# Kernel optimization log

Hardware: AMD Instinct MI355X
Metric: run time of the kernel (lower is better)

## Reference

```python
import jax, jax.numpy as jnp
import numpy as np

N, R, M, E, NE, B = 50000, 500, 120000, 960000, 800000, 8192
D, H1, HID, OC = 200, 256, 512, 50


def setup_inputs() -> dict:
    key = jax.random.key(0)
    ks = jax.random.split(key, 26)
    s = 0.05
    rn = lambda k, shp: jax.random.normal(k, shp, jnp.float32) * s
    return {
        "entity_emb": jax.random.normal(ks[0], (N, D), jnp.float32),
        "rel_emb": jax.random.normal(ks[1], (R, D), jnp.float32),
        "b_x": jax.random.randint(ks[2], (M,), 0, N),
        "b_node_graph_index": jax.random.randint(ks[3], (M,), 0, R),
        "edge_src": jax.random.randint(ks[4], (E,), 0, M),
        "edge_dst": jax.random.randint(ks[5], (E,), 0, M),
        "edge_w": jax.random.uniform(ks[6], (E,), jnp.float32),
        "big_src": jax.random.randint(ks[7], (NE,), 0, N),
        "big_dst": jax.random.randint(ks[8], (NE,), 0, N),
        "big_w": jax.random.uniform(ks[9], (NE,), jnp.float32),
        "perm": jax.random.permutation(ks[10], N),
        "batch_inputs": jnp.stack([
            jax.random.randint(ks[11], (B,), 0, N),
            jax.random.randint(ks[12], (B,), 0, R),
            jax.random.randint(ks[13], (B,), 0, N)], axis=1),
        "W1a": rn(ks[14], (2 * D, H1)), "W1b": rn(ks[15], (H1, D)),
        "W2a": rn(ks[16], (D, H1)), "W2b": rn(ks[17], (H1, D)),
        "Wle": rn(ks[18], (2 * D, 1)), "ble": jnp.zeros((1,), jnp.float32),
        "Wlo": rn(ks[19], (2 * D, D)), "blo": jnp.zeros((D,), jnp.float32),
        "Wg": rn(ks[20], (D, HID)), "Wd": rn(ks[21], (HID, HID)),
        "conv_w": rn(ks[22], (OC, 3)), "conv_b": jnp.zeros((OC,), jnp.float32),
        "fc_w": rn(ks[23], (OC * D, 1)), "fc_b": jnp.zeros((1,), jnp.float32),
    }


def _l2norm(x):
    return x / jnp.maximum(jnp.linalg.norm(x, axis=-1, keepdims=True), 1e-12)


def _gcn(x, src, dst, w, n, Wa, Wb):
    # two-layer GCN over sparse edge list: out = A @ relu(A @ x @ Wa) @ Wb
    agg = lambda h: jax.ops.segment_sum(h[src] * w[:, None], dst, num_segments=n)
    h = jax.nn.relu(agg(x) @ Wa)
    return agg(h) @ Wb


def _seg_softmax(v, idx, n):
    m = jax.ops.segment_max(v, idx, num_segments=n)
    e = jnp.exp(v - m[idx])
    s = jax.ops.segment_sum(e, idx, num_segments=n)
    return e / (s[idx] + 1e-16)


def _mce(ent, rel, b_x, b_gi, src, dst, w, W1a, W1b, Wle, ble, Wlo, blo):
    x = jnp.concatenate([ent[b_x], rel[b_gi]], axis=-1)          # [M, 400]
    e = _gcn(x, src, dst, w, b_x.shape[0], W1a, W1b)             # [M, 200]
    cnt = jax.ops.segment_sum(jnp.ones((b_x.shape[0],), e.dtype), b_x, num_segments=N)
    mean = jax.ops.segment_sum(e, b_x, num_segments=N) / jnp.maximum(cnt, 1.0)[:, None]
    z = mean[b_x]                                                # scatter_mean then gather
    emb = jnp.concatenate([e[b_x], z], axis=-1)                  # [M, 400]
    score = emb @ Wle + ble                                      # [M, 1]
    zs = _seg_softmax(score, b_x, N)                             # segment softmax
    pooled = jax.ops.segment_sum(zs * emb, b_x, num_segments=N)  # [N, 400]
    return (pooled @ Wlo + blo) + ent


def _dgi(h1, h2, Wg, Wd):
    p1 = jax.nn.relu(h1 @ Wg)
    p2 = jax.nn.relu(h2 @ Wg)
    c = jax.nn.sigmoid(jnp.mean(p1, axis=0))                     # readout [HID]
    t = Wd @ c
    return jnp.concatenate([p1 @ t, p2 @ t])                     # [2N]


def _convkb(trip, conv_w, conv_b, fc_w, fc_b):
    # trip [B,3,D]; Conv2d(1, OC, (1,3)) over [B,1,D,3] -> [B,OC,D]
    h = jax.nn.relu(jnp.einsum('bsd,os->bod', trip, conv_w) + conv_b[None, :, None])
    return h.reshape(trip.shape[0], -1) @ fc_w + fc_b            # [B,1]


def reference(entity_emb, rel_emb, b_x, b_node_graph_index, edge_src, edge_dst,
              edge_w, big_src, big_dst, big_w, perm, batch_inputs,
              W1a, W1b, W2a, W2b, Wle, ble, Wlo, blo, Wg, Wd,
              conv_w, conv_b, fc_w, fc_b):
    ent = _l2norm(entity_emb)
    rel = _l2norm(rel_emb)
    ent_shuf = ent[perm]
    ec = _mce(ent, rel, b_x, b_node_graph_index, edge_src, edge_dst, edge_w,
              W1a, W1b, Wle, ble, Wlo, blo)
    ec_ = _mce(ent_shuf, rel, b_x, b_node_graph_index, edge_src, edge_dst, edge_w,
               W1a, W1b, Wle, ble, Wlo, blo)
    eg = _gcn(ec, big_src, big_dst, big_w, N, W2a, W2b)
    eg_ = _gcn(ec_, big_src, big_dst, big_w, N, W2a, W2b)
    local_logits = _dgi(ec, ec_, Wg, Wd)
    global_logits = _dgi(eg, eg_, Wg, Wd)
    trip = jnp.stack([ec[batch_inputs[:, 0]], rel[batch_inputs[:, 1]],
                      ec[batch_inputs[:, 2]]], axis=1)           # [B,3,D]
    out_conv = _convkb(trip, conv_w, conv_b, fc_w, fc_b)
    return out_conv, local_logits, global_logits
```

## Files before the change

### kernel.cpp

```cpp
#include <hip/hip_runtime.h>

#define NN   50000
#define RR   500
#define MM   120000
#define EE   960000
#define NEE  800000
#define BB   8192
#define DD   200
#define HH1  256
#define HIDD 512
#define OCC  50

typedef unsigned int  u32;
typedef unsigned short u16;
typedef __attribute__((ext_vector_type(8))) short bf16x8;
typedef __attribute__((ext_vector_type(4))) float f32x4;

static __device__ __forceinline__ float bf2f(u16 u) {
    u32 x = ((u32)u) << 16;
    return __uint_as_float(x);
}
static __device__ __forceinline__ u16 f2bf(float f) {
    u32 x = __float_as_uint(f);
    u32 r = (x + 0x7FFFu + ((x >> 16) & 1u)) >> 16;
    return (u16)r;
}
static __device__ __forceinline__ u32 pack2(float a, float b) {
    return (u32)f2bf(a) | ((u32)f2bf(b) << 16);
}
static __device__ __forceinline__ void unpack2(u32 v, float& a, float& b) {
    a = bf2f((u16)(v & 0xFFFFu));
    b = bf2f((u16)(v >> 16));
}

static __device__ __forceinline__ float wredsum(float v) {
#pragma unroll
    for (int off = 32; off > 0; off >>= 1) v += __shfl_xor(v, off);
    return v;
}

static __device__ __forceinline__ u32 relu2bf(u32 x) {
    if (x & 0x00008000u) x &= 0xFFFF0000u;
    if (x & 0x80000000u) x &= 0x0000FFFFu;
    return x;
}
static __device__ __forceinline__ bf16x8 zero8() {
    bf16x8 z;
#pragma unroll
    for (int i = 0; i < 8; ++i) z[i] = 0;
    return z;
}

__global__ void k_l2norm(const float* __restrict__ in, float* __restrict__ outf,
                         u16* __restrict__ outb, int rows) {
    int w = (blockIdx.x * blockDim.x + threadIdx.x) >> 6;
    int lane = threadIdx.x & 63;
    if (w >= rows) return;
    const float* r = in + (size_t)w * DD;
    float s = 0.f;
    for (int d = lane; d < DD; d += 64) { float v = r[d]; s += v * v; }
    s = wredsum(s);
    float inv = 1.0f / fmaxf(sqrtf(s), 1e-12f);
    for (int d = lane; d < DD; d += 64) {
        float v = r[d] * inv;
        if (outf) outf[(size_t)w * DD + d] = v;
        if (outb) outb[(size_t)w * DD + d] = f2bf(v);
    }
}

__global__ void k_gather_perm(const int* __restrict__ bx, const int* __restrict__ perm,
                              int* __restrict__ idx1, int M) {
    int m = blockIdx.x * blockDim.x + threadIdx.x;
    if (m < M) idx1[m] = perm[bx[m]];
}

__global__ void k_edge_idx(const int* __restrict__ srcE, const int* __restrict__ map,
                           int* __restrict__ outE, int n) {
    int e = blockIdx.x * blockDim.x + threadIdx.x;
    if (e < n) outE[e] = map[srcE[e]];
}

__global__ void k_prepw(const float* __restrict__ src, int Nc, int Kd,
                        u16* __restrict__ hi, u16* __restrict__ lo) {
    int i = blockIdx.x * blockDim.x + threadIdx.x;
    if (i >= Nc * Kd) return;
    int n = i / Kd, k = i - n * Kd;
    float b = src[(size_t)k * Nc + n];
    u16 hb_ = f2bf(b);
    hi[i] = hb_;
    lo[i] = f2bf(b - bf2f(hb_));
}

__global__ void k_fusew(const float* __restrict__ W2b, const float* __restrict__ Wg,
                        u16* __restrict__ hi, u16* __restrict__ lo) {
    int i = blockIdx.x * blockDim.x + threadIdx.x;
    if (i >= HIDD * HH1) return;
    int n = i >> 8, k = i & 255;
    float s = 0.f;
    for (int j = 0; j < DD; ++j) s += W2b[k * DD + j] * Wg[(size_t)j * HIDD + n];
    u16 h = f2bf(s);
    hi[i] = h;
    lo[i] = f2bf(s - bf2f(h));
}

__global__ void k_hist(const int* __restrict__ idx, int* __restrict__ cnt, int n) {
    int i = blockIdx.x * blockDim.x + threadIdx.x;
    if (i < n) atomicAdd(&cnt[idx[i]], 1);
}

__global__ __launch_bounds__(1024) void k_scan3(
    const int* __restrict__ in0, int* __restrict__ out0, int n0,
    const int* __restrict__ in1, int* __restrict__ out1, int n1,
    const int* __restrict__ in2, int* __restrict__ out2, int n2) {
    __shared__ int wtot[16];
    __shared__ int wexc[16];
    __shared__ int s_carry;
    const int* in = (blockIdx.x == 0) ? in0 : (blockIdx.x == 1) ? in1 : in2;
    int* out = (blockIdx.x == 0) ? out0 : (blockIdx.x == 1) ? out1 : out2;
    int n = (blockIdx.x == 0) ? n0 : (blockIdx.x == 1) ? n1 : n2;
    int tid = threadIdx.x, lane = tid & 63, wid = tid >> 6;
    if (tid == 0) s_carry = 0;
    __syncthreads();
    for (int base = 0; base < n; base += 1024) {
        int i = base + tid;
        int v = (i < n) ? in[i] : 0;
        int x = v;
#pragma unroll
        for (int off = 1; off < 64; off <<= 1) {
            int t = __shfl_up(x, off);
            if (lane >= off) x += t;
        }
        if (lane == 63) wtot[wid] = x;
        __syncthreads();
        if (wid == 0) {
            int wv2 = (lane < 16) ? wtot[lane] : 0;
            int y = wv2;
#pragma unroll
            for (int off = 1; off < 16; off <<= 1) {
                int t = __shfl_up(y, off);
                if (lane >= off) y += t;
            }
            if (lane < 16) wexc[lane] = y - wv2;
            if (lane == 15) wtot[15] = y;
        }
        __syncthreads();
        if (i < n) out[i] = s_carry + wexc[wid] + (x - v);
        int chunk_total = wtot[15];
        __syncthreads();
        if (tid == 0) s_carry += chunk_total;
        __syncthreads();
    }
    if (threadIdx.x == 0) out[n] = s_carry;
}

__global__ void k_fill2(const int* __restrict__ dst, const int* __restrict__ src,
                        const float* __restrict__ w, int* __restrict__ cursor,
                        int* __restrict__ srcs_out, float* __restrict__ ws_out, int n) {
    int e = blockIdx.x * blockDim.x + threadIdx.x;
    if (e >= n) return;
    int p = atomicAdd(&cursor[dst[e]], 1);
    srcs_out[p] = src[e];
    ws_out[p] = w[e];
}

__global__ void k_fill1(const int* __restrict__ idx, int* __restrict__ cursor,
                        int* __restrict__ outm, int n) {
    int m = blockIdx.x * blockDim.x + threadIdx.x;
    if (m >= n) return;
    int p = atomicAdd(&cursor[idx[m]], 1);
    outm[p] = m;
}

__global__ void k_pull_mce(const int* __restrict__ rp, const int* __restrict__ ivE,
                           const int* __restrict__ giE, const float* __restrict__ wE,
                           const u16* __restrict__ Pent, const u16* __restrict__ Prel,
                           u16* __restrict__ out, int ndst) {
    int wv = (blockIdx.x * blockDim.x + threadIdx.x) >> 6;
    if (wv >= ndst) return;
    int lane = threadIdx.x & 63;
    int beg = rp[wv], end = rp[wv + 1];
    float accA[2] = {0.f, 0.f}, accB[2] = {0.f, 0.f};
    int e = beg;
    for (; e + 4 <= end; e += 4) {
        int i0 = ivE[e], i1 = ivE[e + 1], i2 = ivE[e + 2], i3 = ivE[e + 3];
        int g0 = giE[e], g1 = giE[e + 1], g2 = giE[e + 2], g3 = giE[e + 3];
        float w0 = wE[e], w1 = wE[e + 1], w2 = wE[e + 2], w3 = wE[e + 3];
        const u32* pe0 = (const u32*)(Pent + (size_t)i0 * HH1);
        const u32* pe1 = (const u32*)(Pent + (size_t)i1 * HH1);
        const u32* pe2 = (const u32*)(Pent + (size_t)i2 * HH1);
        const u32* pe3 = (const u32*)(Pent + (size_t)i3 * HH1);
        const u32* pr0 = (const u32*)(Prel + (size_t)g0 * HH1);
        const u32* pr1 = (const u32*)(Prel + (size_t)g1 * HH1);
        const u32* pr2 = (const u32*)(Prel + (size_t)g2 * HH1);
        const u32* pr3 = (const u32*)(Prel + (size_t)g3 * HH1);
        u32 vp[4][2], vr[4][2];
#pragma unroll
        for (int t = 0; t < 2; ++t) {
            int p = lane + 64 * t;
            vp[0][t] = pe0[p]; vp[1][t] = pe1[p]; vp[2][t] = pe2[p]; vp[3][t] = pe3[p];
            vr[0][t] = pr0[p]; vr[1][t] = pr1[p]; vr[2][t] = pr2[p]; vr[3][t] = pr3[p];
        }
#pragma unroll
        for (int t = 0; t < 2; ++t) {
            float a, b, c, d;
            unpack2(vp[0][t], a, b); unpack2(vr[0][t], c, d);
            accA[t] += (a + c) * w0; accB[t] += (b + d) * w0;
            unpack2(vp[1][t], a, b); unpack2(vr[1][t], c, d);
            accA[t] += (a + c) * w1; accB[t] += (b + d) * w1;
            unpack2(vp[2][t], a, b); unpack2(vr[2][t], c, d);
            accA[t] += (a + c) * w2; accB[t] += (b + d) * w2;
            unpack2(vp[3][t], a, b); unpack2(vr[3][t], c, d);
            accA[t] += (a + c) * w3; accB[t] += (b + d) * w3;
        }
    }
    for (; e < end; ++e) {
        int iv = ivE[e], gi = giE[e];
        float w = wE[e];
        const u32* pe = (const u32*)(Pent + (size_t)iv * HH1);
        const u32* pr = (const u32*)(Prel + (size_t)gi * HH1);
#pragma unroll
        for (int t = 0; t < 2; ++t) {
            int p = lane + 64 * t;
            float a, b, c, d;
            unpack2(pe[p], a, b); unpack2(pr[p], c, d);
            accA[t] += (a + c) * w; accB[t] += (b + d) * w;
        }
    }
    u32* o = (u32*)(out + (size_t)wv * HH1);
#pragma unroll
    for (int t = 0; t < 2; ++t) o[lane + 64 * t] = pack2(accA[t], accB[t]);
}

template<int DIMS, int INS, int OUTS>
__global__ void k_pull(const int* __restrict__ rp, const int* __restrict__ srcs,
                       const float* __restrict__ wsrt,
                       const u16* __restrict__ inh, const u16* __restrict__ inl,
                       u16* __restrict__ outh, u16* __restrict__ outl, int ndst) {
    int wv = (blockIdx.x * blockDim.x + threadIdx.x) >> 6;
    if (wv >= ndst) return;
    int lane = threadIdx.x & 63;
    int beg = rp[wv], end = rp[wv + 1];
    constexpr int NP = DIMS / 2;
    constexpr int NT = (NP + 63) / 64;
    float accA[NT], accB[NT];
#pragma unroll
    for (int t = 0; t < NT; ++t) { accA[t] = 0.f; accB[t] = 0.f; }
    int e = beg;
    for (; e + 4 <= end; e += 4) {
        int s0 = srcs[e], s1 = srcs[e + 1], s2 = srcs[e + 2], s3 = srcs[e + 3];
        float w0 = wsrt[e], w1 = wsrt[e + 1], w2 = wsrt[e + 2], w3 = wsrt[e + 3];
        const u32* rh[4] = {
            (const u32*)(inh + (size_t)s0 * DIMS), (const u32*)(inh + (size_t)s1 * DIMS),
            (const u32*)(inh + (size_t)s2 * DIMS), (const u32*)(inh + (size_t)s3 * DIMS)};
        u32 vh[4][NT], vl[4][NT];
#pragma unroll
        for (int t = 0; t < NT; ++t) {
            int p = lane + 64 * t;
            if (p < NP) {
                vh[0][t] = rh[0][p]; vh[1][t] = rh[1][p];
                vh[2][t] = rh[2][p]; vh[3][t] = rh[3][p];
            }
        }
        if (INS) {
            const u32* rl[4] = {
                (const u32*)(inl + (size_t)s0 * DIMS), (const u32*)(inl + (size_t)s1 * DIMS),
                (const u32*)(inl + (size_t)s2 * DIMS), (const u32*)(inl + (size_t)s3 * DIMS)};
#pragma unroll
            for (int t = 0; t < NT; ++t) {
                int p = lane + 64 * t;
                if (p < NP) {
                    vl[0][t] = rl[0][p]; vl[1][t] = rl[1][p];
                    vl[2][t] = rl[2][p]; vl[3][t] = rl[3][p];
                }
            }
        }
        float ws[4] = {w0, w1, w2, w3};
#pragma unroll
        for (int q = 0; q < 4; ++q) {
#pragma unroll
            for (int t = 0; t < NT; ++t) {
                int p = lane + 64 * t;
                if (p < NP) {
                    float a, b;
                    unpack2(vh[q][t], a, b);
                    if (INS) { float a2, b2; unpack2(vl[q][t], a2, b2); a += a2; b += b2; }
                    accA[t] += a * ws[q]; accB[t] += b * ws[q];
                }
            }
        }
    }
    for (; e < end; ++e) {
        int s = srcs[e];
        float w = wsrt[e];
        const u32* rh = (const u32*)(inh + (size_t)s * DIMS);
        const u32* rl = INS ? (const u32*)(inl + (size_t)s * DIMS) : nullptr;
#pragma unroll
        for (int t = 0; t < NT; ++t) {
            int p = lane + 64 * t;
            if (p < NP) {
                float a, b;
                unpack2(rh[p], a, b);
                if (INS) { float a2, b2; unpack2(rl[p], a2, b2); a += a2; b += b2; }
                accA[t] += a * w; accB[t] += b * w;
            }
        }
    }
    u32* oh = (u32*)(outh + (size_t)wv * DIMS);
    u32* ol = OUTS ? (u32*)(outl + (size_t)wv * DIMS) : nullptr;
#pragma unroll
    for (int t = 0; t < NT; ++t) {
        int p = lane + 64 * t;
        if (p < NP) {
            if (OUTS == 0) {
                oh[p] = pack2(accA[t], accB[t]);
            } else {
                u16 ha = f2bf(accA[t]), hb_ = f2bf(accB[t]);
                u16 la = f2bf(accA[t] - bf2f(ha)), lb = f2bf(accB[t] - bf2f(hb_));
                oh[p] = (u32)ha | ((u32)hb_ << 16);
                ol[p] = (u32)la | ((u32)lb << 16);
            }
        }
    }
}

__global__ void k_segpool(const int* __restrict__ rpX, const int* __restrict__ mids,
                          const u16* __restrict__ e_buf, u16* __restrict__ pooled, int n) {
    int nv = (blockIdx.x * blockDim.x + threadIdx.x) >> 6;
    if (nv >= n) return;
    int lane = threadIdx.x & 63;
    int beg = rpX[nv], end = rpX[nv + 1];
    int cnt = end - beg;
    float accA[2] = {0.f, 0.f}, accB[2] = {0.f, 0.f};
    int e = beg;
    for (; e + 4 <= end; e += 4) {
        const u32* r0 = (const u32*)(e_buf + (size_t)mids[e] * DD);
        const u32* r1 = (const u32*)(e_buf + (size_t)mids[e + 1] * DD);
        const u32* r2 = (const u32*)(e_buf + (size_t)mids[e + 2] * DD);
        const u32* r3 = (const u32*)(e_buf + (size_t)mids[e + 3] * DD);
        u32 v[4][2];
#pragma unroll
        for (int t = 0; t < 2; ++t) {
            int p = lane + 64 * t;
            if (p < DD / 2) { v[0][t] = r0[p]; v[1][t] = r1[p]; v[2][t] = r2[p]; v[3][t] = r3[p]; }
        }
#pragma unroll
        for (int t = 0; t < 2; ++t) {
            int p = lane + 64 * t;
            if (p < DD / 2) {
                float a, b;
                unpack2(v[0][t], a, b); accA[t] += a; accB[t] += b;
                unpack2(v[1][t], a, b); accA[t] += a; accB[t] += b;
                unpack2(v[2][t], a, b); accA[t] += a; accB[t] += b;
                unpack2(v[3][t], a, b); accA[t] += a; accB[t] += b;
            }
        }
    }
    for (; e < end; ++e) {
        const u32* r = (const u32*)(e_buf + (size_t)mids[e] * DD);
#pragma unroll
        for (int t = 0; t < 2; ++t) {
            int p = lane + 64 * t;
            if (p < DD / 2) { float a, b; unpack2(r[p], a, b); accA[t] += a; accB[t] += b; }
        }
    }
    float inv = 1.0f / fmaxf((float)cnt, 1.0f);
    bool occ = cnt > 0;
    const u32* er = (const u32*)(e_buf + (size_t)nv * DD);
    u32* p0 = (u32*)(pooled + (size_t)nv * (2 * DD));
#pragma unroll
    for (int t = 0; t < 2; ++t) {
        int p = lane + 64 * t;
        if (p < DD / 2) {
            p0[p] = occ ? er[p] : 0u;
            p0[DD / 2 + p] = occ ? pack2(accA[t] * inv, accB[t] * inv) : 0u;
        }
    }
}

template<int AMODE, int BLO, int RELU_IN, int RELU_OUT, int HAS_BIAS, int HAS_ADD, int FUSE, int CMODE>
__global__ __launch_bounds__(256) void k_mfmamm(
    const u16* __restrict__ Ah, const u16* __restrict__ Al,
    const u16* __restrict__ Bh, const u16* __restrict__ Bl,
    void* __restrict__ Cv, u16* __restrict__ Cl,
    int Mr, int Nc, int Kd, int redrows,
    const float* __restrict__ bias, const u16* __restrict__ addsrc,
    const int* __restrict__ addidx, const float* __restrict__ tvec,
    float* __restrict__ redout) {
    constexpr int BM = 128, BK = 32;
    constexpr int ASTR = 40;
    __shared__ u16 Ahs[2][BM * ASTR];
    __shared__ u16 Als[AMODE ? 2 : 1][AMODE ? (BM * ASTR) : 8];

    int tid = threadIdx.x;
    int wid = tid >> 6, lane = tid & 63;
    int wr = wid >> 1, wc = wid & 1;
    int r = lane & 15, h = lane >> 4;
    int bm0 = blockIdx.y * BM, bn0 = blockIdx.x * 128;
    int srow = (tid & 15) + 16 * (tid >> 6);
    int sg = (tid >> 4) & 3;
    int nk = (Kd + BK - 1) / BK;

    f32x4 acc[4][4];
#pragma unroll
    for (int i = 0; i < 4; ++i)
#pragma unroll
        for (int j = 0; j < 4; ++j) acc[i][j] = (f32x4){0.f, 0.f, 0.f, 0.f};

    uint4 pa[2], pl[2];
    {
        int kc = sg * 8;
        bool kok = (kc + 8 <= Kd);
#pragma unroll
        for (int it = 0; it < 2; ++it) {
            int row = srow + 64 * it;
            int gr = bm0 + row;
            uint4 v = make_uint4(0, 0, 0, 0), vl2 = make_uint4(0, 0, 0, 0);
            if (gr < Mr && kok) {
                v = *(const uint4*)(Ah + (size_t)gr * Kd + kc);
                if (AMODE) vl2 = *(const uint4*)(Al + (size_t)gr * Kd + kc);
            }
            if (RELU_IN) {
                v.x = relu2bf(v.x); v.y = relu2bf(v.y);
                v.z = relu2bf(v.z); v.w = relu2bf(v.w);
            }
            pa[it] = v;
            if (AMODE) pl[it] = vl2;
        }
#pragma unroll
        for (int it = 0; it < 2; ++it) {
            int row = srow + 64 * it;
            *(uint4*)(&Ahs[0][row * ASTR + sg * 8]) = pa[it];
            if (AMODE) *(uint4*)(&Als[0][row * ASTR + sg * 8]) = pl[it];
        }
    }
    __syncthreads();

    for (int k = 0; k < nk; ++k) {
        int cur = k & 1;
        uint4 na[2], nl[2];
        bool have_next = (k + 1 < nk);
        if (have_next) {
            int kc = (k + 1) * BK + sg * 8;
            bool kok = (kc + 8 <= Kd);
#pragma unroll
            for (int it = 0; it < 2; ++it) {
                int row = srow + 64 * it;
                int gr = bm0 + row;
                uint4 v = make_uint4(0, 0, 0, 0), vl2 = make_uint4(0, 0, 0, 0);
                if (gr < Mr && kok) {
                    v = *(const uint4*)(Ah + (size_t)gr * Kd + kc);
                    if (AMODE) vl2 = *(const uint4*)(Al + (size_t)gr * Kd + kc);
                }
                if (RELU_IN) {
                    v.x = relu2bf(v.x); v.y = relu2bf(v.y);
                    v.z = relu2bf(v.z); v.w = relu2bf(v.w);
                }
                na[it] = v;
                if (AMODE) nl[it] = vl2;
            }
        }
        bf16x8 bh4[4], bl4[4];
        {
            int kb = k * BK + h * 8;
            bool kbok = (kb + 8 <= Kd);
#pragma unroll
            for (int j = 0; j < 4; ++j) {
                int nrow = bn0 + wc * 64 + j * 16 + r;
                if (nrow < Nc && kbok) {
                    bh4[j] = *(const bf16x8*)(Bh + (size_t)nrow * Kd + kb);
                    if (BLO) bl4[j] = *(const bf16x8*)(Bl + (size_t)nrow * Kd + kb);
                } else { bh4[j] = zero8(); if (BLO) bl4[j] = zero8(); }
            }
        }
        bf16x8 af[4], alr[4];
#pragma unroll
        for (int i = 0; i < 4; ++i) {
            int mrow = wr * 64 + i * 16 + r;
            af[i] = *(const bf16x8*)(&Ahs[cur][mrow * ASTR + h * 8]);
            if (AMODE) alr[i] = *(const bf16x8*)(&Als[cur][mrow * ASTR + h * 8]);
        }
#pragma unroll
        for (int i = 0; i < 4; ++i)
#pragma unroll
            for (int j = 0; j < 4; ++j) {
                acc[i][j] = __builtin_amdgcn_mfma_f32_16x16x32_bf16(af[i], bh4[j], acc[i][j], 0, 0, 0);
                if (BLO)
                    acc[i][j] = __builtin_amdgcn_mfma_f32_16x16x32_bf16(af[i], bl4[j], acc[i][j], 0, 0, 0);
                if (AMODE)
                    acc[i][j] = __builtin_amdgcn_mfma_f32_16x16x32_bf16(alr[i], bh4[j], acc[i][j], 0, 0, 0);
            }
        if (have_next) {
#pragma unroll
            for (int it = 0; it < 2; ++it) {
                int row = srow + 64 * it;
                *(uint4*)(&Ahs[cur ^ 1][row * ASTR + sg * 8]) = na[it];
                if (AMODE) *(uint4*)(&Als[cur ^ 1][row * ASTR + sg * 8]) = nl[it];
            }
        }
        __syncthreads();
    }
    float colacc[4] = {0.f, 0.f, 0.f, 0.f};
#pragma unroll
    for (int i = 0; i < 4; ++i) {
        float rowacc[4] = {0.f, 0.f, 0.f, 0.f};
#pragma unroll
        for (int j = 0; j < 4; ++j) {
            int col = bn0 + wc * 64 + j * 16 + r;
            bool colok = col < Nc;
            float tv = (FUSE == 2 && colok) ? tvec[col] : 0.f;
#pragma unroll
            for (int rg = 0; rg < 4; ++rg) {
                int row = bm0 + wr * 64 + i * 16 + h * 4 + rg;
                float v = acc[i][j][rg];
                if (HAS_BIAS && colok) v += bias[col];
                if (RELU_OUT) v = fmaxf(v, 0.f);
                bool ok = colok && row < Mr;
                if (HAS_ADD && ok) {
                    int r2 = addidx ? addidx[row] : row;
                    v += bf2f(addsrc[(size_t)r2 * Nc + col]);
                }
                if (FUSE != 2 && ok) {
                    size_t cidx = (size_t)row * Nc + col;
                    if (CMODE == 0) ((u16*)Cv)[cidx] = f2bf(v);
                    else if (CMODE == 1) ((float*)Cv)[cidx] = v;
                    else {
                        u16 hi_ = f2bf(v);
                        ((u16*)Cv)[cidx] = hi_;
                        Cl[cidx] = f2bf(v - bf2f(hi_));
                    }
                }
                if (FUSE == 1 && ok && row < redrows) colacc[j] += v;
                if (FUSE == 2) rowacc[rg] += v * tv;
            }
        }
        if (FUSE == 2) {
#pragma unroll
            for (int rg = 0; rg < 4; ++rg) {
                float val = rowacc[rg];
                val += __shfl_xor(val, 1); val += __shfl_xor(val, 2);
                val += __shfl_xor(val, 4); val += __shfl_xor(val, 8);
                int row = bm0 + wr * 64 + i * 16 + h * 4 + rg;
                if (r == 0 && row < Mr) atomicAdd(&redout[row], val);
            }
        }
    }
    if (FUSE == 1) {
#pragma unroll
        for (int j = 0; j < 4; ++j) {
            float val = colacc[j];
            val += __shfl_xor(val, 16); val += __shfl_xor(val, 32);
            int col = bn0 + wc * 64 + j * 16 + r;
            if (h == 0 && col < Nc) atomicAdd(&redout[col], val);
        }
    }
}

__global__ void k_tmv(const float* __restrict__ Wd, const float* __restrict__ csum,
                      float* __restrict__ tvec) {
    __shared__ float c[HIDD];
    int lane = threadIdx.x;
    for (int j = lane; j < HIDD; j += 64)
        c[j] = 1.0f / (1.0f + expf(-csum[j] * (1.0f / (float)NN)));
    __syncthreads();
    int r0 = blockIdx.x * 16;
    for (int i = r0; i < r0 + 16; ++i) {
        const float* wr = Wd + (size_t)i * HIDD;
        float s = 0.f;
        for (int j = lane; j < HIDD; j += 64) s += wr[j] * c[j];
        s = wredsum(s);
        if (lane == 0) tvec[i] = s;
    }
}

__global__ void k_rowdot512(const float* __restrict__ p, const float* __restrict__ t,
                            float* __restrict__ out, int rows) {
    int g = blockIdx.x * blockDim.x + threadIdx.x;
    int wv = g >> 6;
    if (wv >= rows) return;
    int lane = g & 63;
    const float* r = p + (size_t)wv * HIDD;
    float s = 0.f;
#pragma unroll
    for (int t4 = 0; t4 < 8; ++t4) {
        int d = lane + t4 * 64;
        s += r[d] * t[d];
    }
    s = wredsum(s);
    if (lane == 0) out[wv] = s;
}

__global__ void k_rowdot512b(const u16* __restrict__ p, const float* __restrict__ t,
                             float* __restrict__ out, int rows) {
    int g = blockIdx.x * blockDim.x + threadIdx.x;
    int wv = g >> 6;
    if (wv >= rows) return;
    int lane = g & 63;
    const u32* r = (const u32*)(p + (size_t)wv * HIDD);
    float s = 0.f;
#pragma unroll
    for (int t4 = 0; t4 < 4; ++t4) {
        int pp = lane + t4 * 64;
        float a, b;
        unpack2(r[pp], a, b);
        s += a * t[2 * pp] + b * t[2 * pp + 1];
    }
    s = wredsum(s);
    if (lane == 0) out[wv] = s;
}

__global__ void k_convkb(const u16* __restrict__ ec, const float* __restrict__ rel,
                         const int* __restrict__ bi, const float* __restrict__ cw,
                         const float* __restrict__ cb, const float* __restrict__ fcw,
                         const float* __restrict__ fcb, float* __restrict__ out) {
    __shared__ float t0[DD], t1[DD], t2[DD];
    __shared__ float red[4];
    int b = blockIdx.x, tid = threadIdx.x;
    int i0 = bi[b * 3 + 0], i1 = bi[b * 3 + 1], i2 = bi[b * 3 + 2];
    if (tid < DD) {
        t0[tid] = bf2f(ec[(size_t)i0 * DD + tid]);
        t1[tid] = rel[(size_t)i1 * DD + tid];
        t2[tid] = bf2f(ec[(size_t)i2 * DD + tid]);
    }
    __syncthreads();
    float partial = 0.f;
    if (tid < DD) {
        float a = t0[tid], bb = t1[tid], c = t2[tid];
        for (int o = 0; o < OCC; ++o) {
            float h = fmaxf(cw[o * 3 + 0] * a + cw[o * 3 + 1] * bb + cw[o * 3 + 2] * c + cb[o], 0.f);
            partial += h * fcw[o * DD + tid];
        }
    }
    partial = wredsum(partial);
    if ((tid & 63) == 0) red[tid >> 6] = partial;
    __syncthreads();
    if (tid == 0) out[b] = red[0] + red[1] + red[2] + red[3] + fcb[0];
}

__global__ void k_sentinel(float* out, float val) { out[threadIdx.x] = val; }

extern "C" void kernel_launch(void* const* d_in, const int* in_sizes, int n_in,
                              void* d_out, int out_size, void* d_ws, size_t ws_size,
                              hipStream_t stream) {
    const float* entity_emb = (const float*)d_in[0];
    const float* rel_emb    = (const float*)d_in[1];
    const int*   b_x        = (const int*)d_in[2];
    const int*   b_gi       = (const int*)d_in[3];
    const int*   e_src      = (const int*)d_in[4];
    const int*   e_dst      = (const int*)d_in[5];
    const float* e_w        = (const float*)d_in[6];
    const int*   big_src    = (const int*)d_in[7];
    const int*   big_dst    = (const int*)d_in[8];
    const float* big_w      = (const float*)d_in[9];
    const int*   perm       = (const int*)d_in[10];
    const int*   batch_in   = (const int*)d_in[11];
    const float* W1a        = (const float*)d_in[12];
    const float* W1b        = (const float*)d_in[13];
    const float* W2a        = (const float*)d_in[14];
    const float* W2b        = (const float*)d_in[15];
    const float* Wlo        = (const float*)d_in[18];
    const float* blo        = (const float*)d_in[19];
    const float* Wg         = (const float*)d_in[20];
    const float* Wd         = (const float*)d_in[21];
    const float* conv_w     = (const float*)d_in[22];
    const float* conv_b     = (const float*)d_in[23];
    const float* fc_w       = (const float*)d_in[24];
    const float* fc_b       = (const float*)d_in[25];
    float* out = (float*)d_out;

    size_t off = 0;
    auto balloc = [&](size_t nbytes) {
        size_t p = off;
        off += (nbytes + 511) & ~(size_t)511;
        return p;
    };
    char* base = (char*)d_ws;
    u16*   entb = (u16*)(base + balloc((size_t)NN * DD * 2));
    float* relf = (float*)(base + balloc((size_t)RR * DD * 4));
    u16*   relb = (u16*)(base + balloc((size_t)RR * DD * 2));
    u16*   Pent = (u16*)(base + balloc((size_t)NN * HH1 * 2));
    u16*   Prel = (u16*)(base + balloc((size_t)RR * HH1 * 2));
    int*   idx1 = (int*)(base + balloc((size_t)MM * 4));
    int*   rpB  = (int*)(base + balloc((size_t)(NN + 1) * 4));
    int*   srcB = (int*)(base + balloc((size_t)NEE * 4));
    float* wB   = (float*)(base + balloc((size_t)NEE * 4));
    int*   rpE  = (int*)(base + balloc((size_t)(MM + 1) * 4));
    int*   srcE = (int*)(base + balloc((size_t)EE * 4));
    float* wE   = (float*)(base + balloc((size_t)EE * 4));
    int*   ivE  = (int*)(base + balloc((size_t)EE * 4));
    int*   giE  = (int*)(base + balloc((size_t)EE * 4));
    int*   rpX  = (int*)(base + balloc((size_t)(NN + 1) * 4));
    int*   mids = (int*)(base + balloc((size_t)MM * 4));
    int*   curB = (int*)(base + balloc((size_t)NN * 4));
    int*   curE = (int*)(base + balloc((size_t)MM * 4));
    int*   curX = (int*)(base + balloc((size_t)NN * 4));
    u16* w1aT_h  = (u16*)(base + balloc(200 * 256 * 2));
    u16* w1aT_l  = (u16*)(base + balloc(200 * 256 * 2));
    u16* w1abT_h = (u16*)(base + balloc(200 * 256 * 2));
    u16* w1abT_l = (u16*)(base + balloc(200 * 256 * 2));
    u16* w1bT_h  = (u16*)(base + balloc(256 * 200 * 2));
    u16* w1bT_l  = (u16*)(base + balloc(256 * 200 * 2));
    u16* wloT_h  = (u16*)(base + balloc(400 * 200 * 2));
    u16* wloT_l  = (u16*)(base + balloc(400 * 200 * 2));
    u16* wgT_h   = (u16*)(base + balloc(200 * 512 * 2));
    u16* wgT_l   = (u16*)(base + balloc(200 * 512 * 2));
    u16* w2aT_h  = (u16*)(base + balloc(200 * 256 * 2));
    u16* w2aT_l  = (u16*)(base + balloc(200 * 256 * 2));
    u16* w2bgT_h = (u16*)(base + balloc(512 * 256 * 2));
    u16* w2bgT_l = (u16*)(base + balloc(512 * 256 * 2));
    char*  Aarena = base + balloc((size_t)MM * HH1 * 2);
    char*  Barena = base + balloc((size_t)MM * DD * 2);
    char*  Carena = base + balloc((size_t)MM * DD * 2);
    float* csum = (float*)(base + balloc(4 * 2048));
    float* cvec = csum + 512;
    float* t_l  = csum + 1024;
    float* t_g  = csum + 1536;
    u16*   ecb  = (u16*)(base + balloc((size_t)NN * DD * 2));
    size_t off_small = off;
    u16*   ecb2 = ecb + (size_t)NN * DD;
    bool bigws = (off_small + (size_t)NN * DD * 2) <= ws_size;
    (void)cvec;

    if (ws_size < off_small) {
        k_sentinel<<<dim3(1), dim3(8), 0, stream>>>(out, (float)(ws_size >> 20));
        return;
    }

    const size_t PL = 20000000;
    const size_t PH = 25600000;
    u16*   aggx   = (u16*)Aarena;
    u16*   hb     = (u16*)Barena;
    u16*   e_buf  = (u16*)Carena;
    u16*   pooled = (u16*)Aarena;
    u16*   a1h    = (u16*)Aarena;
    u16*   a1l    = (u16*)(Aarena + PL);
    u16*   h2h    = (u16*)Barena;
    u16*   h2l    = (u16*)(Barena + PH);
    u16*   g2h    = (u16*)Aarena;
    u16*   g2l    = (u16*)(Aarena + PH);
    u16*   pb16   = (u16*)Barena;
    u16*   pb16L  = (u16*)Aarena;
    float* pbuf   = (float*)Aarena;

    dim3 blk(256);
    auto wgrid = [](int items) { return dim3((unsigned)((items + 3) / 4)); };
    auto tgrid = [](int items) { return dim3((unsigned)((items + 255) / 256)); };
    auto mmgrid = [](int Mr, int Nc) { return dim3((unsigned)((Nc + 127) / 128), (unsigned)((Mr + 127) / 128)); };

    k_l2norm<<<wgrid(NN), blk, 0, stream>>>(entity_emb, nullptr, entb, NN);
    k_l2norm<<<wgrid(RR), blk, 0, stream>>>(rel_emb, relf, relb, RR);
    k_gather_perm<<<tgrid(MM), blk, 0, stream>>>(b_x, perm, idx1, MM);
    k_prepw<<<tgrid(256 * 200), blk, 0, stream>>>(W1a, 256, 200, w1aT_h, w1aT_l);
    k_prepw<<<tgrid(256 * 200), blk, 0, stream>>>(W1a + 200 * 256, 256, 200, w1abT_h, w1abT_l);
    k_prepw<<<tgrid(200 * 256), blk, 0, stream>>>(W1b, 200, 256, w1bT_h, w1bT_l);
    k_prepw<<<tgrid(200 * 400), blk, 0, stream>>>(Wlo, 200, 400, wloT_h, wloT_l);
    k_prepw<<<tgrid(512 * 200), blk, 0, stream>>>(Wg, 512, 200, wgT_h, wgT_l);
    k_prepw<<<tgrid(256 * 200), blk, 0, stream>>>(W2a, 256, 200, w2aT_h, w2aT_l);
    k_fusew<<<tgrid(512 * 256), blk, 0, stream>>>(W2b, Wg, w2bgT_h, w2bgT_l);

    hipMemsetAsync(curB, 0, (size_t)NN * 4, stream);
    hipMemsetAsync(curE, 0, (size_t)MM * 4, stream);
    hipMemsetAsync(curX, 0, (size_t)NN * 4, stream);
    k_hist<<<tgrid(NEE), blk, 0, stream>>>(big_dst, curB, NEE);
    k_hist<<<tgrid(EE), blk, 0, stream>>>(e_dst, curE, EE);
    k_hist<<<tgrid(MM), blk, 0, stream>>>(b_x, curX, MM);
    k_scan3<<<dim3(3), dim3(1024), 0, stream>>>(curB, rpB, NN, curE, rpE, MM, curX, rpX, NN);
    hipMemcpyAsync(curB, rpB, (size_t)NN * 4, hipMemcpyDeviceToDevice, stream);
    hipMemcpyAsync(curE, rpE, (size_t)MM * 4, hipMemcpyDeviceToDevice, stream);
    hipMemcpyAsync(curX, rpX, (size_t)NN * 4, hipMemcpyDeviceToDevice, stream);
    k_fill2<<<tgrid(NEE), blk, 0, stream>>>(big_dst, big_src, big_w, curB, srcB, wB, NEE);
    k_fill2<<<tgrid(EE), blk, 0, stream>>>(e_dst, e_src, e_w, curE, srcE, wE, EE);
    k_fill1<<<tgrid(MM), blk, 0, stream>>>(b_x, curX, mids, MM);
    k_edge_idx<<<tgrid(EE), blk, 0, stream>>>(srcE, b_gi, giE, EE);

    k_mfmamm<0, 0, 0, 0, 0, 0, 0, 0><<<mmgrid(NN, HH1), blk, 0, stream>>>(
        entb, nullptr, w1aT_h, w1aT_l, Pent, nullptr, NN, HH1, DD, NN,
        nullptr, nullptr, nullptr, nullptr, nullptr);
    k_mfmamm<0, 0, 0, 0, 0, 0, 0, 0><<<mmgrid(RR, HH1), blk, 0, stream>>>(
        relb, nullptr, w1abT_h, w1abT_l, Prel, nullptr, RR, HH1, DD, RR,
        nullptr, nullptr, nullptr, nullptr, nullptr);

    auto mce_pass = [&](int v, u16* ecdst) {
        const int* ivmap  = v ? idx1 : b_x;
        const int* addidx = v ? perm : nullptr;
        k_edge_idx<<<tgrid(EE), blk, 0, stream>>>(srcE, ivmap, ivE, EE);
        k_pull_mce<<<wgrid(MM), blk, 0, stream>>>(rpE, ivE, giE, wE, Pent, Prel, aggx, MM);
        k_mfmamm<0, 0, 1, 0, 0, 0, 0, 0><<<mmgrid(MM, DD), blk, 0, stream>>>(
            aggx, nullptr, w1bT_h, w1bT_l, hb, nullptr, MM, DD, HH1, MM,
            nullptr, nullptr, nullptr, nullptr, nullptr);
        k_pull<DD, 0, 0><<<wgrid(MM), blk, 0, stream>>>(rpE, srcE, wE, hb, nullptr,
                                                        e_buf, nullptr, MM);
        k_segpool<<<wgrid(NN), blk, 0, stream>>>(rpX, mids, e_buf, pooled, NN);
        k_mfmamm<0, 0, 0, 0, 1, 1, 0, 0><<<mmgrid(NN, DD), blk, 0, stream>>>(
            pooled, nullptr, wloT_h, wloT_l, ecdst, nullptr, NN, DD, 2 * DD, NN,
            blo, entb, addidx, nullptr, nullptr);
    };

    auto gcn_pass = [&](int v, const u16* ecsrc) {
        k_pull<DD, 0, 1><<<wgrid(NN), blk, 0, stream>>>(rpB, srcB, wB, ecsrc, nullptr,
                                                        a1h, a1l, NN);
        k_mfmamm<1, 1, 0, 1, 0, 0, 0, 2><<<mmgrid(NN, HH1), blk, 0, stream>>>(
            a1h, a1l, w2aT_h, w2aT_l, h2h, h2l, NN, HH1, DD, NN,
            nullptr, nullptr, nullptr, nullptr, nullptr);
        k_pull<HH1, 1, 1><<<wgrid(NN), blk, 0, stream>>>(rpB, srcB, wB, h2h, h2l,
                                                         g2h, g2l, NN);
        if (v == 0) {
            hipMemsetAsync(csum, 0, 512 * sizeof(float), stream);
            k_mfmamm<1, 1, 0, 1, 0, 0, 1, 0><<<mmgrid(NN, HIDD), blk, 0, stream>>>(
                g2h, g2l, w2bgT_h, w2bgT_l, pb16, nullptr, NN, HIDD, HH1, NN,
                nullptr, nullptr, nullptr, nullptr, csum);
            k_tmv<<<dim3(32), dim3(64), 0, stream>>>(Wd, csum, t_g);
            k_rowdot512b<<<wgrid(NN), blk, 0, stream>>>(pb16, t_g, out + BB + 2 * (size_t)NN, NN);
        } else {
            hipMemsetAsync(out + BB + 3 * (size_t)NN, 0, (size_t)NN * 4, stream);
            k_mfmamm<1, 1, 0, 1, 0, 0, 2, 0><<<mmgrid(NN, HIDD), blk, 0, stream>>>(
                g2h, g2l, w2bgT_h, w2bgT_l, nullptr, nullptr, NN, HIDD, HH1, NN,
                nullptr, nullptr, nullptr, t_g, out + BB + 3 * (size_t)NN);
        }
    };

    if (bigws) {
        mce_pass(0, ecb);
        mce_pass(1, ecb2);
        hipMemsetAsync(csum, 0, 512 * sizeof(float), stream);
        k_mfmamm<0, 0, 0, 1, 0, 0, 1, 0><<<mmgrid(2 * NN, HIDD), blk, 0, stream>>>(
            ecb, nullptr, wgT_h, wgT_l, pb16L, nullptr, 2 * NN, HIDD, DD, NN,
            nullptr, nullptr, nullptr, nullptr, csum);
        k_tmv<<<dim3(32), dim3(64), 0, stream>>>(Wd, csum, t_l);
        k_rowdot512b<<<wgrid(2 * NN), blk, 0, stream>>>(pb16L, t_l, out + BB, 2 * NN);
        k_convkb<<<dim3(BB), blk, 0, stream>>>(ecb, relf, batch_in,
                                               conv_w, conv_b, fc_w, fc_b, out);
        gcn_pass(0, ecb);
        gcn_pass(1, ecb2);
    } else {
        for (int v = 0; v < 2; ++v) {
            mce_pass(v, ecb);
            if (v == 0) {
                hipMemsetAsync(csum, 0, 512 * sizeof(float), stream);
                k_mfmamm<0, 0, 0, 1, 0, 0, 1, 1><<<mmgrid(NN, HIDD), blk, 0, stream>>>(
                    ecb, nullptr, wgT_h, wgT_l, pbuf, nullptr, NN, HIDD, DD, NN,
                    nullptr, nullptr, nullptr, nullptr, csum);
                k_tmv<<<dim3(32), dim3(64), 0, stream>>>(Wd, csum, t_l);
                k_rowdot512<<<wgrid(NN), blk, 0, stream>>>(pbuf, t_l, out + BB, NN);
                k_convkb<<<dim3(BB), blk, 0, stream>>>(ecb, relf, batch_in,
                                                       conv_w, conv_b, fc_w, fc_b, out);
            } else {
                hipMemsetAsync(out + BB + NN, 0, (size_t)NN * 4, stream);
                k_mfmamm<0, 0, 0, 1, 0, 0, 2, 1><<<mmgrid(NN, HIDD), blk, 0, stream>>>(
                    ecb, nullptr, wgT_h, wgT_l, nullptr, nullptr, NN, HIDD, DD, NN,
                    nullptr, nullptr, nullptr, t_l, out + BB + NN);
            }
            gcn_pass(v, ecb);
        }
    }

    (void)in_sizes; (void)n_in; (void)out_size;
}
```

Measured before the change: 1.997 ms.

## Parallelize CSR prefix scan and merge histogram and l2norm launches

Replaces the single-block-per-array serial prefix scan with a three-phase multi-block scan (per-chunk scan, tiny block-offset scan, offset add that also writes the cursor copies). This removes the three device-to-device memcpys. It also merges the three histogram kernels and the two l2norm kernels into single launches. The aim is to cut launch overhead and the long serial scan, at the cost of two extra small kernel launches.

```diff
diff --git a/kernel.cpp b/kernel.cpp
--- a/kernel.cpp
+++ b/kernel.cpp
@@ -51,20 +51,26 @@
     return z;
 }
 
-__global__ void k_l2norm(const float* __restrict__ in, float* __restrict__ outf,
-                         u16* __restrict__ outb, int rows) {
+__global__ void k_l2norm2(const float* __restrict__ ent_in, const float* __restrict__ rel_in,
+                          u16* __restrict__ entb, float* __restrict__ relf,
+                          u16* __restrict__ relb) {
     int w = (blockIdx.x * blockDim.x + threadIdx.x) >> 6;
     int lane = threadIdx.x & 63;
-    if (w >= rows) return;
-    const float* r = in + (size_t)w * DD;
+    if (w >= NN + RR) return;
+    bool isent = w < NN;
+    const float* r = isent ? (ent_in + (size_t)w * DD) : (rel_in + (size_t)(w - NN) * DD);
     float s = 0.f;
     for (int d = lane; d < DD; d += 64) { float v = r[d]; s += v * v; }
     s = wredsum(s);
     float inv = 1.0f / fmaxf(sqrtf(s), 1e-12f);
     for (int d = lane; d < DD; d += 64) {
         float v = r[d] * inv;
-        if (outf) outf[(size_t)w * DD + d] = v;
-        if (outb) outb[(size_t)w * DD + d] = f2bf(v);
+        if (isent) {
+            entb[(size_t)w * DD + d] = f2bf(v);
+        } else {
+            relf[(size_t)(w - NN) * DD + d] = v;
+            relb[(size_t)(w - NN) * DD + d] = f2bf(v);
+        }
     }
 }
 
@@ -103,54 +109,102 @@
     lo[i] = f2bf(s - bf2f(h));
 }
 
-__global__ void k_hist(const int* __restrict__ idx, int* __restrict__ cnt, int n) {
+__global__ void k_hist3(const int* __restrict__ i0, int* __restrict__ c0, int n0,
+                        const int* __restrict__ i1, int* __restrict__ c1, int n1,
+                        const int* __restrict__ i2, int* __restrict__ c2, int n2) {
     int i = blockIdx.x * blockDim.x + threadIdx.x;
-    if (i < n) atomicAdd(&cnt[idx[i]], 1);
-}
-
-__global__ __launch_bounds__(1024) void k_scan3(
-    const int* __restrict__ in0, int* __restrict__ out0, int n0,
-    const int* __restrict__ in1, int* __restrict__ out1, int n1,
-    const int* __restrict__ in2, int* __restrict__ out2, int n2) {
+    if (i < n0) { atomicAdd(&c0[i0[i]], 1); return; }
+    i -= n0;
+    if (i < n1) { atomicAdd(&c1[i1[i]], 1); return; }
+    i -= n1;
+    if (i < n2) atomicAdd(&c2[i2[i]], 1);
+}
+
+__global__ __launch_bounds__(1024) void k_scanA(
+    const int* __restrict__ inB, int* __restrict__ outB, int nB_,
+    const int* __restrict__ inE, int* __restrict__ outE, int nE_,
+    const int* __restrict__ inX, int* __restrict__ outX, int nX_,
+    int* __restrict__ bsum) {
+    int arr = blockIdx.y;
+    const int* in = (arr == 0) ? inB : (arr == 1) ? inE : inX;
+    int* out = (arr == 0) ? outB : (arr == 1) ? outE : outX;
+    int n = (arr == 0) ? nB_ : (arr == 1) ? nE_ : nX_;
+    int chunk = blockIdx.x;
+    if (chunk * 4096 >= n) return;
     __shared__ int wtot[16];
     __shared__ int wexc[16];
-    __shared__ int s_carry;
-    const int* in = (blockIdx.x == 0) ? in0 : (blockIdx.x == 1) ? in1 : in2;
-    int* out = (blockIdx.x == 0) ? out0 : (blockIdx.x == 1) ? out1 : out2;
-    int n = (blockIdx.x == 0) ? n0 : (blockIdx.x == 1) ? n1 : n2;
     int tid = threadIdx.x, lane = tid & 63, wid = tid >> 6;
-    if (tid == 0) s_carry = 0;
+    int base = chunk * 4096 + tid * 4;
+    int v0 = (base + 0 < n) ? in[base + 0] : 0;
+    int v1 = (base + 1 < n) ? in[base + 1] : 0;
+    int v2 = (base + 2 < n) ? in[base + 2] : 0;
+    int v3 = (base + 3 < n) ? in[base + 3] : 0;
+    int tsum = v0 + v1 + v2 + v3;
+    int x = tsum;
+#pragma unroll
+    for (int off = 1; off < 64; off <<= 1) {
+        int t = __shfl_up(x, off);
+        if (lane >= off) x += t;
+    }
+    if (lane == 63) wtot[wid] = x;
     __syncthreads();
-    for (int base = 0; base < n; base += 1024) {
-        int i = base + tid;
-        int v = (i < n) ? in[i] : 0;
-        int x = v;
-#pragma unroll
-        for (int off = 1; off < 64; off <<= 1) {
-            int t = __shfl_up(x, off);
-            if (lane >= off) x += t;
-        }
-        if (lane == 63) wtot[wid] = x;
-        __syncthreads();
-        if (wid == 0) {
-            int wv2 = (lane < 16) ? wtot[lane] : 0;
-            int y = wv2;
-#pragma unroll
-            for (int off = 1; off < 16; off <<= 1) {
-                int t = __shfl_up(y, off);
-                if (lane >= off) y += t;
-            }
-            if (lane < 16) wexc[lane] = y - wv2;
-            if (lane == 15) wtot[15] = y;
-        }
-        __syncthreads();
-        if (i < n) out[i] = s_carry + wexc[wid] + (x - v);
-        int chunk_total = wtot[15];
-        __syncthreads();
-        if (tid == 0) s_carry += chunk_total;
-        __syncthreads();
-    }
-    if (threadIdx.x == 0) out[n] = s_carry;
+    if (wid == 0) {
+        int wv = (lane < 16) ? wtot[lane] : 0;
+        int y = wv;
+#pragma unroll
+        for (int off = 1; off < 16; off <<= 1) {
+            int t = __shfl_up(y, off);
+            if (lane >= off) y += t;
+        }
+        if (lane < 16) wexc[lane] = y - wv;
+        if (lane == 15) bsum[arr * 64 + chunk] = y;
+    }
+    __syncthreads();
+    int texcl = (x - tsum) + wexc[wid];
+    if (base + 0 < n) out[base + 0] = texcl;
+    if (base + 1 < n) out[base + 1] = texcl + v0;
+    if (base + 2 < n) out[base + 2] = texcl + v0 + v1;
+    if (base + 3 < n) out[base + 3] = texcl + v0 + v1 + v2;
+}
+
+__global__ void k_scanB(int* __restrict__ bsum, int* __restrict__ boff,
+                        int* __restrict__ tot, int nB_, int nE_, int nX_) {
+    int arr = threadIdx.x;
+    if (arr >= 3) return;
+    int n = (arr == 0) ? nB_ : (arr == 1) ? nE_ : nX_;
+    int nc = (n + 4095) / 4096;
+    int acc = 0;
+    for (int c = 0; c < nc; ++c) {
+        boff[arr * 64 + c] = acc;
+        acc += bsum[arr * 64 + c];
+    }
+    tot[arr] = acc;
+}
+
+__global__ __launch_bounds__(1024) void k_scanC(
+    int* __restrict__ outB, int* __restrict__ curB, int nB_,
+    int* __restrict__ outE, int* __restrict__ curE, int nE_,
+    int* __restrict__ outX, int* __restrict__ curX, int nX_,
+    const int* __restrict__ boff, const int* __restrict__ tot) {
+    int arr = blockIdx.y;
+    int* out = (arr == 0) ? outB : (arr == 1) ? outE : outX;
+    int* cur = (arr == 0) ? curB : (arr == 1) ? curE : curX;
+    int n = (arr == 0) ? nB_ : (arr == 1) ? nE_ : nX_;
+    int chunk = blockIdx.x;
+    if (chunk * 4096 >= n) return;
+    int off = boff[arr * 64 + chunk];
+    int tid = threadIdx.x;
+    int base = chunk * 4096 + tid * 4;
+#pragma unroll
+    for (int j = 0; j < 4; ++j) {
+        int i = base + j;
+        if (i < n) {
+            int v = out[i] + off;
+            out[i] = v;
+            cur[i] = v;
+        }
+    }
+    if (chunk == 0 && tid == 0) out[n] = tot[arr];
 }
 
 __global__ void k_fill2(const int* __restrict__ dst, const int* __restrict__ src,
@@ -693,6 +747,9 @@
     int*   curB = (int*)(base + balloc((size_t)NN * 4));
     int*   curE = (int*)(base + balloc((size_t)MM * 4));
     int*   curX = (int*)(base + balloc((size_t)NN * 4));
+    int*   bsum = (int*)(base + balloc(192 * 4));
+    int*   boff = (int*)(base + balloc(192 * 4));
+    int*   stot = (int*)(base + balloc(16 * 4));
     u16* w1aT_h  = (u16*)(base + balloc(200 * 256 * 2));
     u16* w1aT_l  = (u16*)(base + balloc(200 * 256 * 2));
     u16* w1abT_h = (u16*)(base + balloc(200 * 256 * 2));
@@ -746,8 +803,7 @@
     auto tgrid = [](int items) { return dim3((unsigned)((items + 255) / 256)); };
     auto mmgrid = [](int Mr, int Nc) { return dim3((unsigned)((Nc + 127) / 128), (unsigned)((Mr + 127) / 128)); };
 
-    k_l2norm<<<wgrid(NN), blk, 0, stream>>>(entity_emb, nullptr, entb, NN);
-    k_l2norm<<<wgrid(RR), blk, 0, stream>>>(rel_emb, relf, relb, RR);
+    k_l2norm2<<<wgrid(NN + RR), blk, 0, stream>>>(entity_emb, rel_emb, entb, relf, relb);
     k_gather_perm<<<tgrid(MM), blk, 0, stream>>>(b_x, perm, idx1, MM);
     k_prepw<<<tgrid(256 * 200), blk, 0, stream>>>(W1a, 256, 200, w1aT_h, w1aT_l);
     k_prepw<<<tgrid(256 * 200), blk, 0, stream>>>(W1a + 200 * 256, 256, 200, w1abT_h, w1abT_l);
@@ -760,13 +816,16 @@
     hipMemsetAsync(curB, 0, (size_t)NN * 4, stream);
     hipMemsetAsync(curE, 0, (size_t)MM * 4, stream);
     hipMemsetAsync(curX, 0, (size_t)NN * 4, stream);
-    k_hist<<<tgrid(NEE), blk, 0, stream>>>(big_dst, curB, NEE);
-    k_hist<<<tgrid(EE), blk, 0, stream>>>(e_dst, curE, EE);
-    k_hist<<<tgrid(MM), blk, 0, stream>>>(b_x, curX, MM);
-    k_scan3<<<dim3(3), dim3(1024), 0, stream>>>(curB, rpB, NN, curE, rpE, MM, curX, rpX, NN);
-    hipMemcpyAsync(curB, rpB, (size_t)NN * 4, hipMemcpyDeviceToDevice, stream);
-    hipMemcpyAsync(curE, rpE, (size_t)MM * 4, hipMemcpyDeviceToDevice, stream);
-    hipMemcpyAsync(curX, rpX, (size_t)NN * 4, hipMemcpyDeviceToDevice, stream);
+    k_hist3<<<tgrid(NEE + EE + MM), blk, 0, stream>>>(big_dst, curB, NEE,
+                                                      e_dst, curE, EE, b_x, curX, MM);
+    {
+        dim3 sgrid((unsigned)((MM + 4095) / 4096), 3);
+        k_scanA<<<sgrid, dim3(1024), 0, stream>>>(curB, rpB, NN, curE, rpE, MM,
+                                                  curX, rpX, NN, bsum);
+        k_scanB<<<dim3(1), dim3(64), 0, stream>>>(bsum, boff, stot, NN, MM, NN);
+        k_scanC<<<sgrid, dim3(1024), 0, stream>>>(rpB, curB, NN, rpE, curE, MM,
+                                                  rpX, curX, NN, boff, stot);
+    }
     k_fill2<<<tgrid(NEE), blk, 0, stream>>>(big_dst, big_src, big_w, curB, srcB, wB, NEE);
     k_fill2<<<tgrid(EE), blk, 0, stream>>>(e_dst, e_src, e_w, curE, srcE, wE, EE);
     k_fill1<<<tgrid(MM), blk, 0, stream>>>(b_x, curX, mids, MM);
```

Result: faster. 1.883 ms (-5.7%).
